# Kernel tuning notes

Measured on AMD Instinct MI355X. Metric: run time of the kernel, lower is better.

Reference implementation:

```python
import jax, jax.numpy as jnp
import numpy as np

DIM, HEADS, EMB = 768, 16, 1024
DH = DIM // HEADS                 # 48, divisible by 3 for 3D RoPE
T, RES = 3, 24
KT, KH, KW = 3, 5, 5              # neighborhood kernel
MLP = 4 * DIM
EPS = 1e-5


def _ln(x, w=None, b=None):
    m = x.mean(-1, keepdims=True)
    v = x.var(-1, keepdims=True)
    y = (x - m) * jax.lax.rsqrt(v + EPS)
    if w is not None:
        y = y * w + b
    return y


def _rope_cos_sin():
    # 3D axial RoPE: dim_head split into 3 equal chunks (t, h, w axes)
    da = DH // 3
    half = da // 2
    inv = 1.0 / (10000.0 ** (jnp.arange(half, dtype=jnp.float32) * 2.0 / da))
    def ang(n):
        return jnp.arange(n, dtype=jnp.float32)[:, None] * inv[None, :]  # (n, half)
    at, ah, aw = ang(T), ang(RES), ang(RES)
    A = jnp.concatenate([
        jnp.broadcast_to(at[:, None, None, :], (T, RES, RES, half)),
        jnp.broadcast_to(ah[None, :, None, :], (T, RES, RES, half)),
        jnp.broadcast_to(aw[None, None, :, :], (T, RES, RES, half)),
    ], axis=-1).reshape(T * RES * RES, DH // 2)
    return jnp.cos(A), jnp.sin(A)


def _rope(x, cos, sin):  # x: (B, nh, THW, DH); interleaved pair rotation
    x1, x2 = x[..., 0::2], x[..., 1::2]
    o1 = x1 * cos - x2 * sin
    o2 = x1 * sin + x2 * cos
    return jnp.stack([o1, o2], axis=-1).reshape(x.shape)


def _nbr(n, k):
    # NATTEN window: centered, shifted inward at borders (always exactly k neighbors)
    start = jnp.clip(jnp.arange(n) - k // 2, 0, n - k)
    return start[:, None] + jnp.arange(k)  # (n, k)


def setup_inputs():
    key = jax.random.key(0)
    ks = jax.random.split(key, 8)
    r = lambda k, s: jax.random.normal(k, s, dtype=jnp.float32) * 0.02
    return {
        "x": jax.random.normal(ks[0], (T, DIM, RES, RES), dtype=jnp.float32),
        "emb": jax.random.normal(ks[1], (T, EMB), dtype=jnp.float32),
        "w_mod": r(ks[2], (EMB, 2 * DIM)),
        "b_mod": jnp.zeros((2 * DIM,), jnp.float32),
        "qn_w": jnp.ones((DH,), jnp.float32),
        "qn_b": jnp.zeros((DH,), jnp.float32),
        "kn_w": jnp.ones((DH,), jnp.float32),
        "kn_b": jnp.zeros((DH,), jnp.float32),
        "W_fused": r(ks[3], (DIM, 3 * DIM + MLP)),
        "b_fused": jnp.zeros((3 * DIM + MLP,), jnp.float32),
        "W_out": r(ks[4], (DIM, DIM)),
        "W_mlp": r(ks[5], (MLP, DIM)),
        "b_mlp": jnp.zeros((DIM,), jnp.float32),
    }


def reference(x, emb, w_mod, b_mod, qn_w, qn_b, kn_w, kn_b,
              W_fused, b_fused, W_out, W_mlp, b_mlp):
    B = x.shape[0] // T
    H = W = RES
    THW = T * H * W
    x5 = x.reshape(B, T, DIM, H, W)
    skip = jnp.transpose(x5, (0, 1, 3, 4, 2))          # (B,T,H,W,C)
    xf = skip.reshape(B, THW, DIM)
    # conditioning emb repeated over spatial positions
    embr = jnp.repeat(emb.reshape(B, T, EMB)[:, :, None, :], H * W, axis=2)
    embr = embr.reshape(B, THW, EMB)
    # NormalizeWithCond: LayerNorm (no affine) + AdaLN modulation from emb
    mod = jax.nn.silu(embr) @ w_mod + b_mod
    scale, shift = jnp.split(mod, 2, axis=-1)
    h = _ln(xf) * (1.0 + scale) + shift
    # fused QKV + MLP projection
    fused = h @ W_fused + b_fused
    qkv, mlp_h = fused[..., :3 * DIM], fused[..., 3 * DIM:]
    qkv = qkv.reshape(B, THW, 3, HEADS, DH).transpose(2, 0, 3, 1, 4)  # (3,B,nh,THW,d)
    q, k, v = qkv[0], qkv[1], qkv[2]
    q = _ln(q, qn_w, qn_b)
    k = _ln(k, kn_w, kn_b)
    cos, sin = _rope_cos_sin()
    q = _rope(q, cos, sin)
    k = _rope(k, cos, sin)
    q = q.reshape(B, HEADS, T, H, W, DH) * (DH ** -0.5)
    k = k.reshape(B, HEADS, T, H, W, DH)
    v = v.reshape(B, HEADS, T, H, W, DH)
    it, ih, iw = _nbr(T, KT), _nbr(H, KH), _nbr(W, KW)
    def gather(z):  # -> (B,nh,T,KT,H,KH,W,KW,d)
        return z[:, :, it][:, :, :, :, ih][:, :, :, :, :, :, iw]
    kg, vg = gather(k), gather(v)
    attn = jnp.einsum('bnthwd,bntahcwed->bnthwace', q, kg)
    attn = jax.nn.softmax(attn.reshape(B, HEADS, T, H, W, KT * KH * KW), axis=-1)
    attn = attn.reshape(B, HEADS, T, H, W, KT, KH, KW)
    xa = jnp.einsum('bnthwace,bntahcwed->bnthwd', attn, vg)
    xa = jnp.transpose(xa, (0, 2, 3, 4, 1, 5)).reshape(B, T, H, W, DIM)
    y = skip + xa @ W_out
    y = y.reshape(B, THW, DIM) + (jax.nn.silu(mlp_h) @ W_mlp + b_mlp)
    y = jnp.transpose(y.reshape(B, T, H, W, DIM), (0, 1, 4, 2, 3))
    return y.reshape(B * T, DIM, H, W)
```

## Files before the change

kernel.cpp:

```cpp
#include <hip/hip_runtime.h>
#include <hip/hip_bf16.h>
#include <math.h>

#define T_    3
#define RES_  24
#define DIM_  768
#define HEADS_ 16
#define DH_   48
#define EMB_  1024
#define HW_   576
#define THW_  1728
#define MP_   1792
#define MLP_  3072
#define NF_   5376
#define QKV_  2304
#define QK_   1536
#define KTOT_ 3840
#define SPLITK_ 6
#define EPS_  1e-5f

typedef __attribute__((ext_vector_type(8))) short bf16x8;
typedef __attribute__((ext_vector_type(4))) float f32x4;

__device__ __forceinline__ float siluf(float x) { return x / (1.f + expf(-x)); }

__device__ __forceinline__ unsigned short f2bf(float f) {
    __hip_bfloat16 b = __float2bfloat16(f);
    return *reinterpret_cast<unsigned short*>(&b);
}

__device__ __forceinline__ float bf2f(unsigned short u) {
    return __uint_as_float(((unsigned)u) << 16);
}

__device__ __forceinline__ void async_copy16(const void* g, void* l) {
    __builtin_amdgcn_global_load_lds(
        (__attribute__((address_space(1))) void*)g,
        (__attribute__((address_space(3))) void*)l,
        16, 0, 0);
}

__global__ __launch_bounds__(256) void conv_wfused_kernel(
    const float* __restrict__ W, unsigned short* __restrict__ Wt)
{
    __shared__ float tile[32][33];
    int n0 = blockIdx.x * 32;
    int k0 = blockIdx.y * 32;
    int c = threadIdx.x & 31;
    int r = threadIdx.x >> 5;
#pragma unroll
    for (int i = 0; i < 4; ++i)
        tile[r + 8 * i][c] = W[(size_t)(k0 + r + 8 * i) * NF_ + n0 + c];
    __syncthreads();
#pragma unroll
    for (int i = 0; i < 4; ++i)
        Wt[(size_t)(n0 + r + 8 * i) * DIM_ + k0 + c] = f2bf(tile[c][r + 8 * i]);
}

__global__ __launch_bounds__(256) void conv_wcat_kernel(
    const float* __restrict__ W_out, const float* __restrict__ W_mlp,
    unsigned short* __restrict__ Wt)
{
    __shared__ float tile[32][33];
    int k0 = blockIdx.x * 32;
    int n0 = blockIdx.y * 32;
    int c = threadIdx.x & 31;
    int r = threadIdx.x >> 5;
#pragma unroll
    for (int i = 0; i < 4; ++i) {
        int k = k0 + r + 8 * i;
        float v = (k < DIM_) ? W_out[(size_t)k * DIM_ + n0 + c]
                             : W_mlp[(size_t)(k - DIM_) * DIM_ + n0 + c];
        tile[r + 8 * i][c] = v;
    }
    __syncthreads();
#pragma unroll
    for (int i = 0; i < 4; ++i)
        Wt[(size_t)(n0 + r + 8 * i) * KTOT_ + k0 + c] = f2bf(tile[c][r + 8 * i]);
}

__global__ __launch_bounds__(256) void mod_kernel(
    const float* __restrict__ emb, const float* __restrict__ w_mod,
    const float* __restrict__ b_mod, float* __restrict__ mod)
{
    int t = blockIdx.y;
    int chunk = blockIdx.x;
    __shared__ float se[EMB_];
    __shared__ float part[128];
    int tid = threadIdx.x;
    for (int i = tid; i < EMB_; i += 256) {
        float e = emb[t * EMB_ + i];
        se[i] = e / (1.f + expf(-e));
    }
    __syncthreads();
    int r = tid >> 7;
    int c = tid & 127;
    int j = chunk * 128 + c;
    const float* wp = w_mod + j;
    float acc = 0.f;
    for (int e = r * 512; e < r * 512 + 512; ++e)
        acc += se[e] * wp[e * 1536];
    if (r == 1) part[c] = acc;
    __syncthreads();
    if (r == 0)
        mod[t * 1536 + j] = acc + part[c] + b_mod[j];
}

__global__ __launch_bounds__(256) void ln_mod_kernel(
    const float* __restrict__ x, const float* __restrict__ mod,
    unsigned short* __restrict__ h)
{
    int m0 = blockIdx.x * 4;
    int t = m0 / HW_;
    int hw0 = m0 - t * HW_;
    const float* xp = x + (size_t)t * DIM_ * HW_ + hw0;
    int tid = threadIdx.x;
    float4 X0 = *(const float4*)(xp + (size_t)tid * HW_);
    float4 X1 = *(const float4*)(xp + (size_t)(tid + 256) * HW_);
    float4 X2 = *(const float4*)(xp + (size_t)(tid + 512) * HW_);
    float4 sv, sqv;
    sv.x = X0.x + X1.x + X2.x;  sv.y = X0.y + X1.y + X2.y;
    sv.z = X0.z + X1.z + X2.z;  sv.w = X0.w + X1.w + X2.w;
    sqv.x = X0.x*X0.x + X1.x*X1.x + X2.x*X2.x;
    sqv.y = X0.y*X0.y + X1.y*X1.y + X2.y*X2.y;
    sqv.z = X0.z*X0.z + X1.z*X1.z + X2.z*X2.z;
    sqv.w = X0.w*X0.w + X1.w*X1.w + X2.w*X2.w;
#pragma unroll
    for (int off = 32; off > 0; off >>= 1) {
        sv.x += __shfl_xor(sv.x, off, 64);  sv.y += __shfl_xor(sv.y, off, 64);
        sv.z += __shfl_xor(sv.z, off, 64);  sv.w += __shfl_xor(sv.w, off, 64);
        sqv.x += __shfl_xor(sqv.x, off, 64); sqv.y += __shfl_xor(sqv.y, off, 64);
        sqv.z += __shfl_xor(sqv.z, off, 64); sqv.w += __shfl_xor(sqv.w, off, 64);
    }
    __shared__ float4 ssum[4], ssq[4];
    int lane = tid & 63, wid = tid >> 6;
    if (lane == 0) { ssum[wid] = sv; ssq[wid] = sqv; }
    __syncthreads();
    float mean[4], rs[4];
#pragma unroll
    for (int j = 0; j < 4; ++j) {
        float tot  = ((const float*)&ssum[0])[j] + ((const float*)&ssum[1])[j]
                   + ((const float*)&ssum[2])[j] + ((const float*)&ssum[3])[j];
        float totq = ((const float*)&ssq[0])[j] + ((const float*)&ssq[1])[j]
                   + ((const float*)&ssq[2])[j] + ((const float*)&ssq[3])[j];
        float mn = tot * (1.f / 768.f);
        float var = totq * (1.f / 768.f) - mn * mn;
        mean[j] = mn;
        rs[j] = rsqrtf(var + EPS_);
    }
    const float* sc = mod + t * 1536;
    const float* sh = sc + 768;
#pragma unroll
    for (int cc = 0; cc < 3; ++cc) {
        int c = tid + cc * 256;
        float4 X = (cc == 0) ? X0 : (cc == 1) ? X1 : X2;
        float scl = 1.f + sc[c];
        float shf = sh[c];
        const float* Xp = (const float*)&X;
#pragma unroll
        for (int j = 0; j < 4; ++j)
            h[(size_t)(m0 + j) * DIM_ + c] =
                f2bf((Xp[j] - mean[j]) * rs[j] * scl + shf);
    }
}

__global__ __launch_bounds__(256) void gemm1_kernel(
    const unsigned short* __restrict__ A,
    const unsigned short* __restrict__ Bt,
    const float* __restrict__ bias,
    float* __restrict__ qkv,
    unsigned short* __restrict__ vb,
    unsigned short* __restrict__ A2)
{
    const int K = DIM_;
    const int NI = K / 32;
    __shared__ unsigned short As[2][128 * 32];
    __shared__ unsigned short Bs[2][64 * 32];
    int tid = threadIdx.x;
    int bm = blockIdx.y * 128;
    int bn = blockIdx.x * 64;
    int wave = tid >> 6, lane = tid & 63;
    int quad = lane >> 4, l16 = lane & 15;
    int wm = (wave & 1) * 64;
    int wn = (wave >> 1) * 32;
    f32x4 acc[4][2] = {};
    int arow0 = tid >> 2,             akoff0 = (tid & 3) * 8;
    int arow1 = (tid + 256) >> 2,     akoff1 = (tid & 3) * 8;
    int brow = tid >> 2,              bkoff = (tid & 3) * 8;
    const unsigned short* Ag0 = A + (size_t)(bm + arow0) * K + akoff0;
    const unsigned short* Ag1 = A + (size_t)(bm + arow1) * K + akoff1;
    const unsigned short* Bg  = Bt + (size_t)(bn + brow) * K + bkoff;
    int la0 = arow0 * 32 + akoff0;
    int la1 = arow1 * 32 + akoff1;
    int lb  = brow * 32 + bkoff;
    async_copy16(Ag0, &As[0][la0]);
    async_copy16(Ag1, &As[0][la1]);
    async_copy16(Bg,  &Bs[0][lb]);
    for (int i = 0; i < NI; ++i) {
        __syncthreads();
        if (i + 1 < NI) {
            int k0 = (i + 1) * 32;
            int b = (i + 1) & 1;
            async_copy16(Ag0 + k0, &As[b][la0]);
            async_copy16(Ag1 + k0, &As[b][la1]);
            async_copy16(Bg + k0,  &Bs[b][lb]);
        }
        int b = i & 1;
        bf16x8 af[4], bf[2];
#pragma unroll
        for (int mt = 0; mt < 4; ++mt)
            af[mt] = *(const bf16x8*)&As[b][(wm + mt * 16 + l16) * 32 + quad * 8];
#pragma unroll
        for (int nt = 0; nt < 2; ++nt)
            bf[nt] = *(const bf16x8*)&Bs[b][(wn + nt * 16 + l16) * 32 + quad * 8];
#pragma unroll
        for (int mt = 0; mt < 4; ++mt)
#pragma unroll
            for (int nt = 0; nt < 2; ++nt)
                acc[mt][nt] = __builtin_amdgcn_mfma_f32_16x16x32_bf16(
                    af[mt], bf[nt], acc[mt][nt], 0, 0, 0);
    }
#pragma unroll
    for (int mt = 0; mt < 4; ++mt) {
#pragma unroll
        for (int nt = 0; nt < 2; ++nt) {
            int gcol = bn + wn + nt * 16 + l16;
            float b = bias[gcol];
#pragma unroll
            for (int r = 0; r < 4; ++r) {
                int grow = bm + wm + mt * 16 + quad * 4 + r;
                if (grow < THW_) {
                    float v = acc[mt][nt][r] + b;
                    if (gcol < QK_)
                        qkv[(size_t)grow * QK_ + gcol] = v;
                    else if (gcol < QKV_)
                        vb[(size_t)grow * DIM_ + (gcol - QK_)] = f2bf(v);
                    else
                        A2[(size_t)grow * KTOT_ + (gcol - QKV_ + DIM_)] = f2bf(siluf(v));
                }
            }
        }
    }
}

__global__ __launch_bounds__(256) void qkln_rope_kernel(
    const float* __restrict__ qkv,
    const float* __restrict__ qn_w, const float* __restrict__ qn_b,
    const float* __restrict__ kn_w, const float* __restrict__ kn_b,
    unsigned short* __restrict__ qb, unsigned short* __restrict__ kb)
{
    int tid = threadIdx.x;
    int lane = tid & 63, wid = tid >> 6;
    int idx = blockIdx.x * 4 + wid;
    int head = idx / THW_;
    int m = idx - head * THW_;
    const float* fp = qkv + (size_t)m * QK_ + head * DH_;
    float qv = 0.f, kv = 0.f;
    if (lane < DH_) { qv = fp[lane]; kv = fp[768 + lane]; }
    float s = qv, sq = qv * qv, sk = kv, sqk = kv * kv;
#pragma unroll
    for (int off = 32; off > 0; off >>= 1) {
        s   += __shfl_xor(s, off, 64);
        sq  += __shfl_xor(sq, off, 64);
        sk  += __shfl_xor(sk, off, 64);
        sqk += __shfl_xor(sqk, off, 64);
    }
    float mq = s  * (1.f / 48.f), vq = sq  * (1.f / 48.f) - mq * mq;
    float mk = sk * (1.f / 48.f), vk = sqk * (1.f / 48.f) - mk * mk;
    float qn = 0.f, kn = 0.f;
    if (lane < DH_) {
        qn = (qv - mq) * rsqrtf(vq + EPS_) * qn_w[lane] + qn_b[lane];
        kn = (kv - mk) * rsqrtf(vk + EPS_) * kn_w[lane] + kn_b[lane];
    }
    int t = m / HW_; int hw = m - t * HW_;
    int hh = hw / RES_; int ww = hw - hh * RES_;
    int i = lane >> 1;
    int grp = i >> 3, j = i & 7;
    float pos = (grp == 0) ? (float)t : (grp == 1) ? (float)hh : (float)ww;
    float invf = exp2f(-1.6609640474436813f * (float)j);
    float ang = pos * invf;
    float cs = cosf(ang), sn = sinf(ang);
    float qp = __shfl_xor(qn, 1, 64);
    float kp = __shfl_xor(kn, 1, 64);
    float qo, ko;
    if ((lane & 1) == 0) { qo = qn * cs - qp * sn; ko = kn * cs - kp * sn; }
    else                 { qo = qp * sn + qn * cs; ko = kp * sn + kn * cs; }
    if (lane < DH_) {
        size_t o = ((size_t)head * THW_ + m) * DH_ + lane;
        qb[o] = f2bf(qo * 0.14433756729740643f);
        kb[o] = f2bf(ko);
    }
}

__global__ __launch_bounds__(256) void attn_kernel(
    const unsigned short* __restrict__ qb, const unsigned short* __restrict__ kb,
    const unsigned short* __restrict__ vb, unsigned short* __restrict__ A2)
{
    __shared__ unsigned short Ks[144 * 72];
    __shared__ unsigned short Vt[48 * 168];
    __shared__ unsigned short Ps[64 * 168];

    int tid = threadIdx.x;
    int lane = tid & 63, wave = tid >> 6;
    int quad = lane >> 4, l16 = lane & 15;

    int head = blockIdx.x / 27;
    int tile = blockIdx.x - head * 27;
    int tt = tile / 9;
    int sp = tile - tt * 9;
    int h0 = (sp / 3) * 8;
    int w0 = (sp - (sp / 3) * 3) * 8;
    int u0h = min(max(h0 - 2, 0), RES_ - 12);
    int u0w = min(max(w0 - 2, 0), RES_ - 12);

    const unsigned short* qbh = qb + (size_t)head * THW_ * DH_;
    const unsigned short* kbh = kb + (size_t)head * THW_ * DH_;
    const unsigned short* vbh = vb + head * DH_;

    for (int i = tid; i < 144 * 24; i += 256) {
        int r = i / 24;
        Ks[r * 72 + 48 + (i - r * 24)] = 0;
    }
    for (int i = tid; i < 48 * 24; i += 256) {
        int r = i / 24;
        Vt[r * 168 + 144 + (i - r * 24)] = 0;
    }
    for (int i = tid; i < 64 * 24; i += 256) {
        int r = i / 24;
        Ps[r * 168 + 144 + (i - r * 24)] = 0;
    }

    int qbase = wave * 16;
    bf16x8 qf0, qf1;
    {
        int g = qbase + l16;
        int qtok = tt * HW_ + (h0 + (g >> 3)) * RES_ + (w0 + (g & 7));
        const unsigned short* qp = qbh + (size_t)qtok * DH_;
        qf0 = *(const bf16x8*)(qp + quad * 8);
        if (quad < 2) qf1 = *(const bf16x8*)(qp + 32 + quad * 8);
        else {
#pragma unroll
            for (int i = 0; i < 8; ++i) qf1[i] = 0;
        }
    }

    int vmask[4];
#pragma unroll
    for (int r = 0; r < 4; ++r) {
        int g = qbase + quad * 4 + r;
        int qh = h0 + (g >> 3), qw = w0 + (g & 7);
        int hs = min(max(qh - 2, 0), RES_ - 5);
        int ws = min(max(qw - 2, 0), RES_ - 5);
        int vm = 0;
#pragma unroll
        for (int nt = 0; nt < 9; ++nt) {
            int kk = nt * 16 + l16;
            int hc = u0h + kk / 12;
            int wc = u0w + kk - (kk / 12) * 12;
            int ok = (hc >= hs) & (hc < hs + 5) & (wc >= ws) & (wc < ws + 5);
            vm |= ok << nt;
        }
        vmask[r] = vm;
    }

    float mrow[4] = {-1e30f, -1e30f, -1e30f, -1e30f};
    float lrow[4] = {};
    f32x4 Oacc[3] = {};

    for (int a = 0; a < T_; ++a) {
        for (int i = tid; i < 144 * 12; i += 256) {
            int kk = i / 12;
            int g = i - kk * 12;
            int hc = u0h + kk / 12;
            int wc = u0w + kk - (kk / 12) * 12;
            int tok = a * HW_ + hc * RES_ + wc;
            ushort4 k4 = *(const ushort4*)(kbh + (size_t)tok * DH_ + 4 * g);
            *(ushort4*)&Ks[kk * 72 + 4 * g] = k4;
            ushort4 v4 = *(const ushort4*)(vbh + (size_t)tok * DIM_ + 4 * g);
            Vt[(4 * g + 0) * 168 + kk] = v4.x;
            Vt[(4 * g + 1) * 168 + kk] = v4.y;
            Vt[(4 * g + 2) * 168 + kk] = v4.z;
            Vt[(4 * g + 3) * 168 + kk] = v4.w;
        }
        __syncthreads();

        f32x4 sc[9];
#pragma unroll
        for (int nt = 0; nt < 9; ++nt) {
            bf16x8 kf0 = *(const bf16x8*)&Ks[(nt * 16 + l16) * 72 + quad * 8];
            bf16x8 kf1 = *(const bf16x8*)&Ks[(nt * 16 + l16) * 72 + 32 + quad * 8];
            f32x4 z = {};
            z = __builtin_amdgcn_mfma_f32_16x16x32_bf16(qf0, kf0, z, 0, 0, 0);
            sc[nt] = __builtin_amdgcn_mfma_f32_16x16x32_bf16(qf1, kf1, z, 0, 0, 0);
        }

        float rmax[4] = {-1e30f, -1e30f, -1e30f, -1e30f};
#pragma unroll
        for (int nt = 0; nt < 9; ++nt)
#pragma unroll
            for (int r = 0; r < 4; ++r) {
                float s = ((vmask[r] >> nt) & 1) ? sc[nt][r] : -1e30f;
                sc[nt][r] = s;
                rmax[r] = fmaxf(rmax[r], s);
            }
#pragma unroll
        for (int off = 1; off < 16; off <<= 1)
#pragma unroll
            for (int r = 0; r < 4; ++r)
                rmax[r] = fmaxf(rmax[r], __shfl_xor(rmax[r], off));
        float alpha[4], rsum[4] = {};
#pragma unroll
        for (int r = 0; r < 4; ++r) {
            float mn = fmaxf(mrow[r], rmax[r]);
            alpha[r] = expf(mrow[r] - mn);
            mrow[r] = mn;
        }
#pragma unroll
        for (int nt = 0; nt < 9; ++nt)
#pragma unroll
            for (int r = 0; r < 4; ++r) {
                float p = expf(sc[nt][r] - mrow[r]);
                rsum[r] += p;
                Ps[(qbase + quad * 4 + r) * 168 + nt * 16 + l16] = f2bf(p);
            }
#pragma unroll
        for (int off = 1; off < 16; off <<= 1)
#pragma unroll
            for (int r = 0; r < 4; ++r)
                rsum[r] += __shfl_xor(rsum[r], off);
#pragma unroll
        for (int r = 0; r < 4; ++r)
            lrow[r] = lrow[r] * alpha[r] + rsum[r];
#pragma unroll
        for (int vt = 0; vt < 3; ++vt)
#pragma unroll
            for (int r = 0; r < 4; ++r)
                Oacc[vt][r] *= alpha[r];

#pragma unroll
        for (int ks = 0; ks < 5; ++ks) {
            bf16x8 pf = *(const bf16x8*)&Ps[(qbase + l16) * 168 + ks * 32 + quad * 8];
#pragma unroll
            for (int vt = 0; vt < 3; ++vt) {
                bf16x8 vf = *(const bf16x8*)&Vt[(vt * 16 + l16) * 168 + ks * 32 + quad * 8];
                Oacc[vt] = __builtin_amdgcn_mfma_f32_16x16x32_bf16(pf, vf, Oacc[vt], 0, 0, 0);
            }
        }
        __syncthreads();
    }

#pragma unroll
    for (int r = 0; r < 4; ++r) {
        int g = qbase + quad * 4 + r;
        int m = tt * HW_ + (h0 + (g >> 3)) * RES_ + (w0 + (g & 7));
        float inv = 1.f / lrow[r];
#pragma unroll
        for (int vt = 0; vt < 3; ++vt) {
            int d = vt * 16 + l16;
            A2[(size_t)m * KTOT_ + head * DH_ + d] = f2bf(Oacc[vt][r] * inv);
        }
    }
}

__global__ __launch_bounds__(256) void gemm2_kernel(
    const unsigned short* __restrict__ A,
    const unsigned short* __restrict__ Bt,
    unsigned short* __restrict__ P)
{
    const int K = KTOT_;
    const int NI = (KTOT_ / SPLITK_) / 32;
    __shared__ unsigned short As[2][128 * 32];
    __shared__ unsigned short Bs[2][64 * 32];
    int tid = threadIdx.x;
    int bm = blockIdx.y * 128;
    int bn = blockIdx.x * 64;
    int ks = blockIdx.z * (KTOT_ / SPLITK_);
    int wave = tid >> 6, lane = tid & 63;
    int quad = lane >> 4, l16 = lane & 15;
    int wm = (wave & 1) * 64;
    int wn = (wave >> 1) * 32;
    f32x4 acc[4][2] = {};
    int arow0 = tid >> 2,         akoff0 = (tid & 3) * 8;
    int arow1 = (tid + 256) >> 2, akoff1 = (tid & 3) * 8;
    int brow = tid >> 2,          bkoff = (tid & 3) * 8;
    const unsigned short* Ag0 = A + (size_t)(bm + arow0) * K + akoff0 + ks;
    const unsigned short* Ag1 = A + (size_t)(bm + arow1) * K + akoff1 + ks;
    const unsigned short* Bg  = Bt + (size_t)(bn + brow) * K + bkoff + ks;
    int la0 = arow0 * 32 + akoff0;
    int la1 = arow1 * 32 + akoff1;
    int lb  = brow * 32 + bkoff;
    async_copy16(Ag0, &As[0][la0]);
    async_copy16(Ag1, &As[0][la1]);
    async_copy16(Bg,  &Bs[0][lb]);
    for (int i = 0; i < NI; ++i) {
        __syncthreads();
        if (i + 1 < NI) {
            int k0 = (i + 1) * 32;
            int b = (i + 1) & 1;
            async_copy16(Ag0 + k0, &As[b][la0]);
            async_copy16(Ag1 + k0, &As[b][la1]);
            async_copy16(Bg + k0,  &Bs[b][lb]);
        }
        int b = i & 1;
        bf16x8 af[4], bf[2];
#pragma unroll
        for (int mt = 0; mt < 4; ++mt)
            af[mt] = *(const bf16x8*)&As[b][(wm + mt * 16 + l16) * 32 + quad * 8];
#pragma unroll
        for (int nt = 0; nt < 2; ++nt)
            bf[nt] = *(const bf16x8*)&Bs[b][(wn + nt * 16 + l16) * 32 + quad * 8];
#pragma unroll
        for (int mt = 0; mt < 4; ++mt)
#pragma unroll
            for (int nt = 0; nt < 2; ++nt)
                acc[mt][nt] = __builtin_amdgcn_mfma_f32_16x16x32_bf16(
                    af[mt], bf[nt], acc[mt][nt], 0, 0, 0);
    }
    unsigned short* Pp = P + (size_t)blockIdx.z * MP_ * DIM_;
#pragma unroll
    for (int mt = 0; mt < 4; ++mt) {
#pragma unroll
        for (int nt = 0; nt < 2; ++nt) {
            int gcol = bn + wn + nt * 16 + l16;
#pragma unroll
            for (int r = 0; r < 4; ++r) {
                int grow = bm + wm + mt * 16 + quad * 4 + r;
                if (grow < THW_)
                    Pp[(size_t)grow * DIM_ + gcol] = f2bf(acc[mt][nt][r]);
            }
        }
    }
}

__global__ __launch_bounds__(256) void reduce_out_kernel(
    const unsigned short* __restrict__ P, const float* __restrict__ x,
    const float* __restrict__ b_mlp, float* __restrict__ out)
{
    __shared__ float tile[32][65];
    int bm = blockIdx.x * 64;
    int bn = blockIdx.y * 32;
    int tid = threadIdx.x;
    int t = bm / HW_;
    int hw0 = bm - t * HW_;
    for (int i = tid; i < 512; i += 256) {
        int ml = i >> 3;
        int n4 = (i & 7) * 4;
        float s0 = 0.f, s1 = 0.f, s2 = 0.f, s3 = 0.f;
#pragma unroll
        for (int sI = 0; sI < SPLITK_; ++sI) {
            const unsigned short* pp =
                P + ((size_t)sI * MP_ + bm + ml) * DIM_ + bn + n4;
            ushort4 u = *(const ushort4*)pp;
            s0 += bf2f(u.x); s1 += bf2f(u.y);
            s2 += bf2f(u.z); s3 += bf2f(u.w);
        }
        tile[n4 + 0][ml] = s0;
        tile[n4 + 1][ml] = s1;
        tile[n4 + 2][ml] = s2;
        tile[n4 + 3][ml] = s3;
    }
    __syncthreads();
    for (int i = tid; i < 512; i += 256) {
        int n = i >> 4;
        int ms = (i & 15) * 4;
        int gn = bn + n;
        size_t base = ((size_t)t * DIM_ + gn) * HW_ + hw0 + ms;
        float bv = b_mlp[gn];
        float4 xv = *(const float4*)(x + base);
        float4 o;
        o.x = xv.x + bv + tile[n][ms + 0];
        o.y = xv.y + bv + tile[n][ms + 1];
        o.z = xv.z + bv + tile[n][ms + 2];
        o.w = xv.w + bv + tile[n][ms + 3];
        *(float4*)(out + base) = o;
    }
}

extern "C" void kernel_launch(void* const* d_in, const int* in_sizes, int n_in,
                              void* d_out, int out_size, void* d_ws, size_t ws_size,
                              hipStream_t stream) {
    const float* x       = (const float*)d_in[0];
    const float* emb     = (const float*)d_in[1];
    const float* w_mod   = (const float*)d_in[2];
    const float* b_mod   = (const float*)d_in[3];
    const float* qn_w    = (const float*)d_in[4];
    const float* qn_b    = (const float*)d_in[5];
    const float* kn_w    = (const float*)d_in[6];
    const float* kn_b    = (const float*)d_in[7];
    const float* W_fused = (const float*)d_in[8];
    const float* b_fused = (const float*)d_in[9];
    const float* W_out   = (const float*)d_in[10];
    const float* W_mlp   = (const float*)d_in[11];
    const float* b_mlp   = (const float*)d_in[12];
    float* out = (float*)d_out;

    char* w = (char*)d_ws;
    float* mod = (float*)w;            w += (size_t)4608 * 4;
    float* qkv = (float*)w;            w += (size_t)THW_ * QK_ * 4;
    unsigned short* vb  = (unsigned short*)w;  w += (size_t)THW_ * DIM_ * 2;
    unsigned short* qb  = (unsigned short*)w;  w += (size_t)HEADS_ * THW_ * DH_ * 2;
    unsigned short* kb  = (unsigned short*)w;  w += (size_t)HEADS_ * THW_ * DH_ * 2;
    unsigned short* h   = (unsigned short*)w;  w += (size_t)MP_ * DIM_ * 2;
    unsigned short* A2  = (unsigned short*)w;  w += (size_t)MP_ * KTOT_ * 2;
    unsigned short* Bt1 = (unsigned short*)w;  w += (size_t)NF_ * DIM_ * 2;
    unsigned short* Bt2 = (unsigned short*)w;  w += (size_t)DIM_ * KTOT_ * 2;
    unsigned short* P   = (unsigned short*)w;  w += (size_t)SPLITK_ * MP_ * DIM_ * 2;

    conv_wfused_kernel<<<dim3(NF_ / 32, DIM_ / 32), 256, 0, stream>>>(W_fused, Bt1);
    conv_wcat_kernel<<<dim3(KTOT_ / 32, DIM_ / 32), 256, 0, stream>>>(W_out, W_mlp, Bt2);
    mod_kernel<<<dim3(12, 3), 256, 0, stream>>>(emb, w_mod, b_mod, mod);
    ln_mod_kernel<<<THW_ / 4, 256, 0, stream>>>(x, mod, h);
    gemm1_kernel<<<dim3(NF_ / 64, MP_ / 128), 256, 0, stream>>>(h, Bt1, b_fused, qkv, vb, A2);
    qkln_rope_kernel<<<(HEADS_ * THW_) / 4, 256, 0, stream>>>(qkv, qn_w, qn_b, kn_w, kn_b, qb, kb);
    attn_kernel<<<HEADS_ * 27, 256, 0, stream>>>(qb, kb, vb, A2);
    gemm2_kernel<<<dim3(DIM_ / 64, MP_ / 128, SPLITK_), 256, 0, stream>>>(A2, Bt2, P);
    reduce_out_kernel<<<dim3(THW_ / 64, DIM_ / 32), 256, 0, stream>>>(P, x, b_mlp, out);
}
```

Measured before the change: 235.1 us.

## Load GEMM operands directly from global memory into registers, dropping LDS staging

Both GEMM kernels no longer stage A and B tiles through double-buffered shared memory with async global-to-LDS copies. Each lane now loads its MFMA fragments straight from global memory, with the k-loop unrolled by two. This removes the LDS round trip and the per-iteration block barrier. In exchange, waves sharing rows or columns load them redundantly from global memory or cache, and there is no explicit prefetch to hide load latency.

New measurement: 323.7 us. 1.38x slower.

```diff
diff --git a/kernel.cpp b/kernel.cpp
--- a/kernel.cpp
+++ b/kernel.cpp
@@ -33,13 +33,6 @@
     return __uint_as_float(((unsigned)u) << 16);
 }
 
-__device__ __forceinline__ void async_copy16(const void* g, void* l) {
-    __builtin_amdgcn_global_load_lds(
-        (__attribute__((address_space(1))) void*)g,
-        (__attribute__((address_space(3))) void*)l,
-        16, 0, 0);
-}
-
 __global__ __launch_bounds__(256) void conv_wfused_kernel(
     const float* __restrict__ W, unsigned short* __restrict__ Wt)
 {
@@ -173,9 +166,6 @@
     unsigned short* __restrict__ A2)
 {
     const int K = DIM_;
-    const int NI = K / 32;
-    __shared__ unsigned short As[2][128 * 32];
-    __shared__ unsigned short Bs[2][64 * 32];
     int tid = threadIdx.x;
     int bm = blockIdx.y * 128;
     int bn = blockIdx.x * 64;
@@ -184,35 +174,23 @@
     int wm = (wave & 1) * 64;
     int wn = (wave >> 1) * 32;
     f32x4 acc[4][2] = {};
-    int arow0 = tid >> 2,             akoff0 = (tid & 3) * 8;
-    int arow1 = (tid + 256) >> 2,     akoff1 = (tid & 3) * 8;
-    int brow = tid >> 2,              bkoff = (tid & 3) * 8;
-    const unsigned short* Ag0 = A + (size_t)(bm + arow0) * K + akoff0;
-    const unsigned short* Ag1 = A + (size_t)(bm + arow1) * K + akoff1;
-    const unsigned short* Bg  = Bt + (size_t)(bn + brow) * K + bkoff;
-    int la0 = arow0 * 32 + akoff0;
-    int la1 = arow1 * 32 + akoff1;
-    int lb  = brow * 32 + bkoff;
-    async_copy16(Ag0, &As[0][la0]);
-    async_copy16(Ag1, &As[0][la1]);
-    async_copy16(Bg,  &Bs[0][lb]);
-    for (int i = 0; i < NI; ++i) {
-        __syncthreads();
-        if (i + 1 < NI) {
-            int k0 = (i + 1) * 32;
-            int b = (i + 1) & 1;
-            async_copy16(Ag0 + k0, &As[b][la0]);
-            async_copy16(Ag1 + k0, &As[b][la1]);
-            async_copy16(Bg + k0,  &Bs[b][lb]);
-        }
-        int b = i & 1;
+    const unsigned short* ap[4];
+    const unsigned short* bp[2];
+#pragma unroll
+    for (int mt = 0; mt < 4; ++mt)
+        ap[mt] = A + (size_t)(bm + wm + mt * 16 + l16) * K + quad * 8;
+#pragma unroll
+    for (int nt = 0; nt < 2; ++nt)
+        bp[nt] = Bt + (size_t)(bn + wn + nt * 16 + l16) * K + quad * 8;
+#pragma unroll 2
+    for (int k0 = 0; k0 < K; k0 += 32) {
         bf16x8 af[4], bf[2];
 #pragma unroll
         for (int mt = 0; mt < 4; ++mt)
-            af[mt] = *(const bf16x8*)&As[b][(wm + mt * 16 + l16) * 32 + quad * 8];
+            af[mt] = *(const bf16x8*)(ap[mt] + k0);
 #pragma unroll
         for (int nt = 0; nt < 2; ++nt)
-            bf[nt] = *(const bf16x8*)&Bs[b][(wn + nt * 16 + l16) * 32 + quad * 8];
+            bf[nt] = *(const bf16x8*)(bp[nt] + k0);
 #pragma unroll
         for (int mt = 0; mt < 4; ++mt)
 #pragma unroll
@@ -468,9 +446,6 @@
     unsigned short* __restrict__ P)
 {
     const int K = KTOT_;
-    const int NI = (KTOT_ / SPLITK_) / 32;
-    __shared__ unsigned short As[2][128 * 32];
-    __shared__ unsigned short Bs[2][64 * 32];
     int tid = threadIdx.x;
     int bm = blockIdx.y * 128;
     int bn = blockIdx.x * 64;
@@ -480,35 +455,23 @@
     int wm = (wave & 1) * 64;
     int wn = (wave >> 1) * 32;
     f32x4 acc[4][2] = {};
-    int arow0 = tid >> 2,         akoff0 = (tid & 3) * 8;
-    int arow1 = (tid + 256) >> 2, akoff1 = (tid & 3) * 8;
-    int brow = tid >> 2,          bkoff = (tid & 3) * 8;
-    const unsigned short* Ag0 = A + (size_t)(bm + arow0) * K + akoff0 + ks;
-    const unsigned short* Ag1 = A + (size_t)(bm + arow1) * K + akoff1 + ks;
-    const unsigned short* Bg  = Bt + (size_t)(bn + brow) * K + bkoff + ks;
-    int la0 = arow0 * 32 + akoff0;
-    int la1 = arow1 * 32 + akoff1;
-    int lb  = brow * 32 + bkoff;
-    async_copy16(Ag0, &As[0][la0]);
-    async_copy16(Ag1, &As[0][la1]);
-    async_copy16(Bg,  &Bs[0][lb]);
-    for (int i = 0; i < NI; ++i) {
-        __syncthreads();
-        if (i + 1 < NI) {
-            int k0 = (i + 1) * 32;
-            int b = (i + 1) & 1;
-            async_copy16(Ag0 + k0, &As[b][la0]);
-            async_copy16(Ag1 + k0, &As[b][la1]);
-            async_copy16(Bg + k0,  &Bs[b][lb]);
-        }
-        int b = i & 1;
+    const unsigned short* ap[4];
+    const unsigned short* bp[2];
+#pragma unroll
+    for (int mt = 0; mt < 4; ++mt)
+        ap[mt] = A + (size_t)(bm + wm + mt * 16 + l16) * K + quad * 8 + ks;
+#pragma unroll
+    for (int nt = 0; nt < 2; ++nt)
+        bp[nt] = Bt + (size_t)(bn + wn + nt * 16 + l16) * K + quad * 8 + ks;
+#pragma unroll 2
+    for (int k0 = 0; k0 < KTOT_ / SPLITK_; k0 += 32) {
         bf16x8 af[4], bf[2];
 #pragma unroll
         for (int mt = 0; mt < 4; ++mt)
-            af[mt] = *(const bf16x8*)&As[b][(wm + mt * 16 + l16) * 32 + quad * 8];
+            af[mt] = *(const bf16x8*)(ap[mt] + k0);
 #pragma unroll
         for (int nt = 0; nt < 2; ++nt)
-            bf[nt] = *(const bf16x8*)&Bs[b][(wn + nt * 16 + l16) * 32 + quad * 8];
+            bf[nt] = *(const bf16x8*)(bp[nt] + k0);
 #pragma unroll
         for (int mt = 0; mt < 4; ++mt)
 #pragma unroll
```

## Merge weight-prep and modulation kernels, store QK in bf16, share attention LDS buffer

Applied to the files above, without the earlier changes.

Merges the two weight transpose/convert kernels and the modulation GEMV into a single launch that picks its role from the block index, removing two kernel launches and their serialization gaps. The Q/K projection output from the first GEMM is now written as bf16 rather than fp32, halving that intermediate's write and read traffic, at the cost of rounding Q/K before layernorm. The attention kernel aliases the K tile and the probability tile in one LDS buffer to cut shared-memory use. This needs an extra barrier and re-zeroing the padding each iteration.

Result: no change. 231.6 us (-1.5%).

```diff
diff --git a/kernel.cpp b/kernel.cpp
--- a/kernel.cpp
+++ b/kernel.cpp
@@ -40,70 +40,68 @@
         16, 0, 0);
 }
 
-__global__ __launch_bounds__(256) void conv_wfused_kernel(
-    const float* __restrict__ W, unsigned short* __restrict__ Wt)
-{
-    __shared__ float tile[32][33];
-    int n0 = blockIdx.x * 32;
-    int k0 = blockIdx.y * 32;
-    int c = threadIdx.x & 31;
-    int r = threadIdx.x >> 5;
-#pragma unroll
-    for (int i = 0; i < 4; ++i)
-        tile[r + 8 * i][c] = W[(size_t)(k0 + r + 8 * i) * NF_ + n0 + c];
-    __syncthreads();
-#pragma unroll
-    for (int i = 0; i < 4; ++i)
-        Wt[(size_t)(n0 + r + 8 * i) * DIM_ + k0 + c] = f2bf(tile[c][r + 8 * i]);
-}
-
-__global__ __launch_bounds__(256) void conv_wcat_kernel(
+__global__ __launch_bounds__(256) void prep_kernel(
+    const float* __restrict__ W_fused, unsigned short* __restrict__ Bt1,
     const float* __restrict__ W_out, const float* __restrict__ W_mlp,
-    unsigned short* __restrict__ Wt)
-{
-    __shared__ float tile[32][33];
-    int k0 = blockIdx.x * 32;
-    int n0 = blockIdx.y * 32;
-    int c = threadIdx.x & 31;
-    int r = threadIdx.x >> 5;
-#pragma unroll
-    for (int i = 0; i < 4; ++i) {
-        int k = k0 + r + 8 * i;
-        float v = (k < DIM_) ? W_out[(size_t)k * DIM_ + n0 + c]
-                             : W_mlp[(size_t)(k - DIM_) * DIM_ + n0 + c];
-        tile[r + 8 * i][c] = v;
-    }
-    __syncthreads();
-#pragma unroll
-    for (int i = 0; i < 4; ++i)
-        Wt[(size_t)(n0 + r + 8 * i) * KTOT_ + k0 + c] = f2bf(tile[c][r + 8 * i]);
-}
-
-__global__ __launch_bounds__(256) void mod_kernel(
+    unsigned short* __restrict__ Bt2,
     const float* __restrict__ emb, const float* __restrict__ w_mod,
     const float* __restrict__ b_mod, float* __restrict__ mod)
 {
-    int t = blockIdx.y;
-    int chunk = blockIdx.x;
-    __shared__ float se[EMB_];
-    __shared__ float part[128];
+    __shared__ float buf[1152];
+    int b = blockIdx.x;
     int tid = threadIdx.x;
-    for (int i = tid; i < EMB_; i += 256) {
-        float e = emb[t * EMB_ + i];
-        se[i] = e / (1.f + expf(-e));
-    }
-    __syncthreads();
-    int r = tid >> 7;
-    int c = tid & 127;
-    int j = chunk * 128 + c;
-    const float* wp = w_mod + j;
-    float acc = 0.f;
-    for (int e = r * 512; e < r * 512 + 512; ++e)
-        acc += se[e] * wp[e * 1536];
-    if (r == 1) part[c] = acc;
-    __syncthreads();
-    if (r == 0)
-        mod[t * 1536 + j] = acc + part[c] + b_mod[j];
+    if (b < 4032) {
+        float (*tile)[33] = (float(*)[33])buf;
+        int n0 = (b % 168) * 32;
+        int k0 = (b / 168) * 32;
+        int c = tid & 31, r = tid >> 5;
+#pragma unroll
+        for (int i = 0; i < 4; ++i)
+            tile[r + 8 * i][c] = W_fused[(size_t)(k0 + r + 8 * i) * NF_ + n0 + c];
+        __syncthreads();
+#pragma unroll
+        for (int i = 0; i < 4; ++i)
+            Bt1[(size_t)(n0 + r + 8 * i) * DIM_ + k0 + c] = f2bf(tile[c][r + 8 * i]);
+    } else if (b < 6912) {
+        int b2 = b - 4032;
+        float (*tile)[33] = (float(*)[33])buf;
+        int k0 = (b2 % 120) * 32;
+        int n0 = (b2 / 120) * 32;
+        int c = tid & 31, r = tid >> 5;
+#pragma unroll
+        for (int i = 0; i < 4; ++i) {
+            int k = k0 + r + 8 * i;
+            float v = (k < DIM_) ? W_out[(size_t)k * DIM_ + n0 + c]
+                                 : W_mlp[(size_t)(k - DIM_) * DIM_ + n0 + c];
+            tile[r + 8 * i][c] = v;
+        }
+        __syncthreads();
+#pragma unroll
+        for (int i = 0; i < 4; ++i)
+            Bt2[(size_t)(n0 + r + 8 * i) * KTOT_ + k0 + c] = f2bf(tile[c][r + 8 * i]);
+    } else {
+        int b3 = b - 6912;
+        int t = b3 / 12;
+        int chunk = b3 - t * 12;
+        float* se = buf;
+        float* part = buf + 1024;
+        for (int i = tid; i < EMB_; i += 256) {
+            float e = emb[t * EMB_ + i];
+            se[i] = e / (1.f + expf(-e));
+        }
+        __syncthreads();
+        int r = tid >> 7;
+        int c = tid & 127;
+        int j = chunk * 128 + c;
+        const float* wp = w_mod + j;
+        float acc = 0.f;
+        for (int e = r * 512; e < r * 512 + 512; ++e)
+            acc += se[e] * wp[e * 1536];
+        if (r == 1) part[c] = acc;
+        __syncthreads();
+        if (r == 0)
+            mod[t * 1536 + j] = acc + part[c] + b_mod[j];
+    }
 }
 
 __global__ __launch_bounds__(256) void ln_mod_kernel(
@@ -168,7 +166,7 @@
     const unsigned short* __restrict__ A,
     const unsigned short* __restrict__ Bt,
     const float* __restrict__ bias,
-    float* __restrict__ qkv,
+    unsigned short* __restrict__ qkvb,
     unsigned short* __restrict__ vb,
     unsigned short* __restrict__ A2)
 {
@@ -232,7 +230,7 @@
                 if (grow < THW_) {
                     float v = acc[mt][nt][r] + b;
                     if (gcol < QK_)
-                        qkv[(size_t)grow * QK_ + gcol] = v;
+                        qkvb[(size_t)grow * QK_ + gcol] = f2bf(v);
                     else if (gcol < QKV_)
                         vb[(size_t)grow * DIM_ + (gcol - QK_)] = f2bf(v);
                     else
@@ -244,7 +242,7 @@
 }
 
 __global__ __launch_bounds__(256) void qkln_rope_kernel(
-    const float* __restrict__ qkv,
+    const unsigned short* __restrict__ qkv,
     const float* __restrict__ qn_w, const float* __restrict__ qn_b,
     const float* __restrict__ kn_w, const float* __restrict__ kn_b,
     unsigned short* __restrict__ qb, unsigned short* __restrict__ kb)
@@ -254,9 +252,9 @@
     int idx = blockIdx.x * 4 + wid;
     int head = idx / THW_;
     int m = idx - head * THW_;
-    const float* fp = qkv + (size_t)m * QK_ + head * DH_;
+    const unsigned short* fp = qkv + (size_t)m * QK_ + head * DH_;
     float qv = 0.f, kv = 0.f;
-    if (lane < DH_) { qv = fp[lane]; kv = fp[768 + lane]; }
+    if (lane < DH_) { qv = bf2f(fp[lane]); kv = bf2f(fp[768 + lane]); }
     float s = qv, sq = qv * qv, sk = kv, sqk = kv * kv;
 #pragma unroll
     for (int off = 32; off > 0; off >>= 1) {
@@ -296,9 +294,8 @@
     const unsigned short* __restrict__ qb, const unsigned short* __restrict__ kb,
     const unsigned short* __restrict__ vb, unsigned short* __restrict__ A2)
 {
-    __shared__ unsigned short Ks[144 * 72];
+    __shared__ unsigned short U[64 * 168];
     __shared__ unsigned short Vt[48 * 168];
-    __shared__ unsigned short Ps[64 * 168];
 
     int tid = threadIdx.x;
     int lane = tid & 63, wave = tid >> 6;
@@ -317,17 +314,9 @@
     const unsigned short* kbh = kb + (size_t)head * THW_ * DH_;
     const unsigned short* vbh = vb + head * DH_;
 
-    for (int i = tid; i < 144 * 24; i += 256) {
-        int r = i / 24;
-        Ks[r * 72 + 48 + (i - r * 24)] = 0;
-    }
     for (int i = tid; i < 48 * 24; i += 256) {
         int r = i / 24;
         Vt[r * 168 + 144 + (i - r * 24)] = 0;
-    }
-    for (int i = tid; i < 64 * 24; i += 256) {
-        int r = i / 24;
-        Ps[r * 168 + 144 + (i - r * 24)] = 0;
     }
 
     int qbase = wave * 16;
@@ -366,6 +355,7 @@
     float mrow[4] = {-1e30f, -1e30f, -1e30f, -1e30f};
     float lrow[4] = {};
     f32x4 Oacc[3] = {};
+    ushort4 z4; z4.x = 0; z4.y = 0; z4.z = 0; z4.w = 0;
 
     for (int a = 0; a < T_; ++a) {
         for (int i = tid; i < 144 * 12; i += 256) {
@@ -375,24 +365,30 @@
             int wc = u0w + kk - (kk / 12) * 12;
             int tok = a * HW_ + hc * RES_ + wc;
             ushort4 k4 = *(const ushort4*)(kbh + (size_t)tok * DH_ + 4 * g);
-            *(ushort4*)&Ks[kk * 72 + 4 * g] = k4;
+            *(ushort4*)&U[kk * 72 + 4 * g] = k4;
             ushort4 v4 = *(const ushort4*)(vbh + (size_t)tok * DIM_ + 4 * g);
             Vt[(4 * g + 0) * 168 + kk] = v4.x;
             Vt[(4 * g + 1) * 168 + kk] = v4.y;
             Vt[(4 * g + 2) * 168 + kk] = v4.z;
             Vt[(4 * g + 3) * 168 + kk] = v4.w;
         }
+        for (int i = tid; i < 144 * 6; i += 256) {
+            int kk = i / 6;
+            int g = i - kk * 6;
+            *(ushort4*)&U[kk * 72 + 48 + 4 * g] = z4;
+        }
         __syncthreads();
 
         f32x4 sc[9];
 #pragma unroll
         for (int nt = 0; nt < 9; ++nt) {
-            bf16x8 kf0 = *(const bf16x8*)&Ks[(nt * 16 + l16) * 72 + quad * 8];
-            bf16x8 kf1 = *(const bf16x8*)&Ks[(nt * 16 + l16) * 72 + 32 + quad * 8];
+            bf16x8 kf0 = *(const bf16x8*)&U[(nt * 16 + l16) * 72 + quad * 8];
+            bf16x8 kf1 = *(const bf16x8*)&U[(nt * 16 + l16) * 72 + 32 + quad * 8];
             f32x4 z = {};
             z = __builtin_amdgcn_mfma_f32_16x16x32_bf16(qf0, kf0, z, 0, 0, 0);
             sc[nt] = __builtin_amdgcn_mfma_f32_16x16x32_bf16(qf1, kf1, z, 0, 0, 0);
         }
+        __syncthreads();
 
         float rmax[4] = {-1e30f, -1e30f, -1e30f, -1e30f};
 #pragma unroll
@@ -421,8 +417,12 @@
             for (int r = 0; r < 4; ++r) {
                 float p = expf(sc[nt][r] - mrow[r]);
                 rsum[r] += p;
-                Ps[(qbase + quad * 4 + r) * 168 + nt * 16 + l16] = f2bf(p);
+                U[(qbase + quad * 4 + r) * 168 + nt * 16 + l16] = f2bf(p);
             }
+        {
+            int rr = lane >> 2, cc = (lane & 3) * 4;
+            *(ushort4*)&U[(qbase + rr) * 168 + 144 + cc] = z4;
+        }
 #pragma unroll
         for (int off = 1; off < 16; off <<= 1)
 #pragma unroll
@@ -439,7 +439,7 @@
 
 #pragma unroll
         for (int ks = 0; ks < 5; ++ks) {
-            bf16x8 pf = *(const bf16x8*)&Ps[(qbase + l16) * 168 + ks * 32 + quad * 8];
+            bf16x8 pf = *(const bf16x8*)&U[(qbase + l16) * 168 + ks * 32 + quad * 8];
 #pragma unroll
             for (int vt = 0; vt < 3; ++vt) {
                 bf16x8 vf = *(const bf16x8*)&Vt[(vt * 16 + l16) * 168 + ks * 32 + quad * 8];
@@ -596,7 +596,7 @@
 
     char* w = (char*)d_ws;
     float* mod = (float*)w;            w += (size_t)4608 * 4;
-    float* qkv = (float*)w;            w += (size_t)THW_ * QK_ * 4;
+    unsigned short* qkv = (unsigned short*)w;  w += (size_t)THW_ * QK_ * 2;
     unsigned short* vb  = (unsigned short*)w;  w += (size_t)THW_ * DIM_ * 2;
     unsigned short* qb  = (unsigned short*)w;  w += (size_t)HEADS_ * THW_ * DH_ * 2;
     unsigned short* kb  = (unsigned short*)w;  w += (size_t)HEADS_ * THW_ * DH_ * 2;
@@ -606,9 +606,8 @@
     unsigned short* Bt2 = (unsigned short*)w;  w += (size_t)DIM_ * KTOT_ * 2;
     unsigned short* P   = (unsigned short*)w;  w += (size_t)SPLITK_ * MP_ * DIM_ * 2;
 
-    conv_wfused_kernel<<<dim3(NF_ / 32, DIM_ / 32), 256, 0, stream>>>(W_fused, Bt1);
-    conv_wcat_kernel<<<dim3(KTOT_ / 32, DIM_ / 32), 256, 0, stream>>>(W_out, W_mlp, Bt2);
-    mod_kernel<<<dim3(12, 3), 256, 0, stream>>>(emb, w_mod, b_mod, mod);
+    prep_kernel<<<6948, 256, 0, stream>>>(W_fused, Bt1, W_out, W_mlp, Bt2,
+                                          emb, w_mod, b_mod, mod);
     ln_mod_kernel<<<THW_ / 4, 256, 0, stream>>>(x, mod, h);
     gemm1_kernel<<<dim3(NF_ / 64, MP_ / 128), 256, 0, stream>>>(h, Bt1, b_fused, qkv, vb, A2);
     qkln_rope_kernel<<<(HEADS_ * THW_) / 4, 256, 0, stream>>>(qkv, qn_w, qn_b, kn_w, kn_b, qb, kb);
```
